# Kernel optimization log

Hardware: AMD Instinct MI355X
Metric: run time of the kernel (lower is better)

Reference implementation:

```python
import jax, jax.numpy as jnp
import numpy as np
from jax import lax

D = 4            # shift radius
NSHIFT = 2 * D + 1  # 9 shifts per axis -> 81 total


def setup_inputs() -> dict:
    key = jax.random.key(0)
    k1, k2, k3, k4, k5, k6 = jax.random.split(key, 6)
    B, C, H, W = 4, 256, 64, 128
    R = 16  # reduction ratio
    feat1 = jax.random.normal(k1, (B, C, H, W), dtype=jnp.float32)
    feat2 = jax.random.normal(k2, (B, C, H, W), dtype=jnp.float32)
    # ca_conv1: Conv2d(C, C//R, 1) -> weight [C//R, C], bias [C//R]
    w1 = jax.random.normal(k3, (C // R, C), dtype=jnp.float32) * (1.0 / np.sqrt(C))
    b1 = jax.random.normal(k4, (C // R,), dtype=jnp.float32) * 0.01
    # ca_conv2: Conv2d(C//R, C, 1) -> weight [C, C//R], bias [C]
    w2 = jax.random.normal(k5, (C, C // R), dtype=jnp.float32) * (1.0 / np.sqrt(C // R))
    b2 = jax.random.normal(k6, (C,), dtype=jnp.float32) * 0.01
    return {"feat1": feat1, "feat2": feat2, "w1": w1, "b1": b1, "w2": w2, "b2": b2}


def reference(feat1, feat2, w1, b1, w2, b2):
    B, C, H, W = feat1.shape
    # zero-pad feat2 spatially by D on each side (matches F.pad constant 0)
    feat2p = jnp.pad(feat2, ((0, 0), (0, 0), (D, D), (D, D)))

    def one_shift(carry, idx):
        i = idx // NSHIFT
        j = idx % NSHIFT
        f2 = lax.dynamic_slice(feat2p, (0, 0, i, j), (B, C, H, W))
        sim = feat1 * f2                              # [B,C,H,W]
        pooled = jnp.mean(sim, axis=(2, 3))           # global avg pool -> [B,C]
        a = pooled @ w1.T + b1                        # [B,C//R] (1x1 conv == matmul)
        a = a @ w2.T + b2                             # [B,C]
        a = jax.nn.sigmoid(a)
        out = jnp.mean(a[:, :, None, None] * sim, axis=1)  # channel mean -> [B,H,W]
        return carry, out

    _, cv = lax.scan(one_shift, None, jnp.arange(NSHIFT * NSHIFT))  # [81,B,H,W]
    return jnp.transpose(cv, (1, 0, 2, 3))  # [B,81,H,W]
```

## Files before the change

kernel.cpp:

```cpp
#include <hip/hip_runtime.h>
#include <math.h>


#define HH 64
#define WW 128
#define CC 256
#define BB 4

__global__ __launch_bounds__(256) void corr_pool_kernel(
    const float* __restrict__ f1, const float* __restrict__ f2,
    float* __restrict__ pooled_part) {
  const int bid   = blockIdx.x;
  const int strip = bid & 1;
  const int bc    = bid >> 1;
  const int h0    = strip << 5;
  const float* f1p = f1 + (size_t)bc * (HH * WW);
  const float* f2p = f2 + (size_t)bc * (HH * WW);

  __shared__ float4 f2s[40 * 35];
  __shared__ float  rowpart[16 * 81];

  const int t = threadIdx.x;
  const float4 z4 = make_float4(0.f, 0.f, 0.f, 0.f);
  for (int u = t; u < 40 * 35; u += 256) {
    const int rl = u / 35, k = u - rl * 35;
    const int gr = h0 - 4 + rl;
    float4 v = z4;
    if ((unsigned)gr < 64u && k >= 1 && k <= 32)
      v = *(const float4*)(f2p + (gr << 7) + ((k - 1) << 2));
    f2s[u] = v;
  }

  const int hl = t >> 3, seg = t & 7, w0 = seg << 4;
  alignas(16) float f1r[16];
#pragma unroll
  for (int m = 0; m < 4; ++m)
    *(float4*)&f1r[4 * m] =
        *(const float4*)(f1p + ((h0 + hl) << 7) + w0 + (m << 2));
  __syncthreads();

  for (int i = 0; i < 9; ++i) {
    alignas(16) float f2r[24];
    const float4* src = &f2s[(hl + i) * 35 + (seg << 2)];
#pragma unroll
    for (int m = 0; m < 6; ++m) *(float4*)&f2r[4 * m] = src[m];

    float s9[9];
#pragma unroll
    for (int j = 0; j < 9; ++j) s9[j] = 0.f;
#pragma unroll
    for (int k = 0; k < 16; ++k) {
      const float a = f1r[k];
#pragma unroll
      for (int j = 0; j < 9; ++j) s9[j] += a * f2r[k + j];
    }
#pragma unroll
    for (int j = 0; j < 9; ++j) {
      s9[j] += __shfl_xor(s9[j], 1);
      s9[j] += __shfl_xor(s9[j], 2);
      s9[j] += __shfl_xor(s9[j], 4);
      s9[j] += __shfl_xor(s9[j], 8);
    }
    if ((t & 15) == 0) {
      const int pr = t >> 4;
#pragma unroll
      for (int j = 0; j < 9; ++j) rowpart[pr * 81 + i * 9 + j] = s9[j];
    }
  }
  __syncthreads();

  if (t < 81) {
    float acc = 0.f;
#pragma unroll
    for (int p = 0; p < 16; ++p) acc += rowpart[p * 81 + t];
    const int b = bc >> 8, c = bc & 255;
    pooled_part[(size_t)strip * 82944 + (size_t)(b * 81 + t) * 256 + c] = acc;
  }
}

__global__ __launch_bounds__(256) void mlp_kernel(
    const float* __restrict__ pooled_part, const float* __restrict__ w1,
    const float* __restrict__ b1, const float* __restrict__ w2,
    const float* __restrict__ b2, float* __restrict__ At) {
  const int bs = blockIdx.x;
  const int t  = threadIdx.x;
  const int b  = bs / 81;
  const int s  = bs - b * 81;
  __shared__ float p[256];
  __shared__ float hid[16];

  p[t] = (pooled_part[(size_t)bs * 256 + t] +
          pooled_part[82944 + (size_t)bs * 256 + t]) * (1.0f / 8192.0f);
  __syncthreads();

  const int g = t >> 4, ln = t & 15;
  float acc = 0.f;
#pragma unroll
  for (int m = 0; m < 16; ++m) {
    const int c = (m << 4) + ln;
    acc += w1[(g << 8) + c] * p[c];
  }
  acc += __shfl_xor(acc, 1);
  acc += __shfl_xor(acc, 2);
  acc += __shfl_xor(acc, 4);
  acc += __shfl_xor(acc, 8);
  if (ln == 0) hid[g] = acc + b1[g];
  __syncthreads();

  float acc2 = b2[t];
#pragma unroll
  for (int k = 0; k < 16; ++k) acc2 += w2[(t << 4) + k] * hid[k];
  const float sv = 1.0f / (1.0f + __expf(-acc2));
  At[((size_t)(b * 256 + t)) * 81 + s] = sv;
}

__global__ __launch_bounds__(64, 4) void out_kernel(
    const float* __restrict__ f1, const float* __restrict__ f2,
    const float* __restrict__ At, float* __restrict__ out,
    float* __restrict__ part) {
  const int bid  = blockIdx.x;
  const int x    = bid & 7;
  const int q    = bid >> 3;
  const int i    = q % 9;
  const int tq   = q / 9;
  const int tile = tq * 8 + x;
  const int half = tile & 1;
  const int rt   = (tile >> 1) & 31;
  const int b    = tile >> 6;
  const int h0   = rt << 1;

  const int t    = threadIdx.x;
  const int r    = t >> 5;
  const int cidx = t & 31;
  const int w0   = cidx << 2;
  const int h    = h0 + r;
  const int hr   = h + i - 4;
  const bool rowok = ((unsigned)hr < 64u);

  float acc[9][4];
#pragma unroll
  for (int j = 0; j < 9; ++j)
#pragma unroll
    for (int k = 0; k < 4; ++k) acc[j][k] = 0.f;

  if (rowok) {
    const int c0 = half << 7;
    const float* p1 = f1 + (size_t)b * (CC * 8192) + (size_t)c0 * 8192 +
                      (h << 7) + w0;
    const float* p2 = f2 + (size_t)b * (CC * 8192) + (size_t)c0 * 8192 +
                      (hr << 7);
    const float* Ab = At + (size_t)b * (CC * 81) + (size_t)c0 * 81 + i * 9;

    const bool vA  = (cidx > 0);
    const bool vC  = (cidx < 31);
    const int ofsA = vA ? (w0 - 4) : 0;
    const int ofsC = vC ? (w0 + 4) : 120;

    float4 nx = *(const float4*)(p1);
    float4 nA = *(const float4*)(p2 + ofsA);
    float4 nB = *(const float4*)(p2 + w0);
    float4 nC = *(const float4*)(p2 + ofsC);

#pragma unroll 4
    for (int c = 0; c < 128; ++c) {
      const float4 xv = nx, fA = nA, fB = nB, fC = nC;
      if (c + 1 < 128) {
        p1 += 8192;
        p2 += 8192;
        nx = *(const float4*)(p1);
        nA = *(const float4*)(p2 + ofsA);
        nB = *(const float4*)(p2 + w0);
        nC = *(const float4*)(p2 + ofsC);
      }

      alignas(16) float f2r[12];
      f2r[0] = vA ? fA.x : 0.f;
      f2r[1] = vA ? fA.y : 0.f;
      f2r[2] = vA ? fA.z : 0.f;
      f2r[3] = vA ? fA.w : 0.f;
      f2r[4] = fB.x; f2r[5] = fB.y; f2r[6] = fB.z; f2r[7] = fB.w;
      f2r[8]  = vC ? fC.x : 0.f;
      f2r[9]  = vC ? fC.y : 0.f;
      f2r[10] = vC ? fC.z : 0.f;
      f2r[11] = vC ? fC.w : 0.f;

      alignas(16) const float xx[4] = {xv.x, xv.y, xv.z, xv.w};

      const float* avp = Ab + (size_t)c * 81;
#pragma unroll
      for (int j = 0; j < 9; ++j) {
        const float wj = avp[j];
#pragma unroll
        for (int k = 0; k < 4; ++k) acc[j][k] += wj * (xx[k] * f2r[k + j]);
      }
    }
  }

  float* dst = half ? part : out;
  const float inv = 1.0f / 256.0f;
#pragma unroll
  for (int j = 0; j < 9; ++j) {
    float4 o;
    o.x = acc[j][0] * inv;
    o.y = acc[j][1] * inv;
    o.z = acc[j][2] * inv;
    o.w = acc[j][3] * inv;
    *(float4*)(dst + (((size_t)(b * 81 + i * 9 + j) * 64 + h) << 7) + w0) = o;
  }
}

__global__ __launch_bounds__(256) void combine_kernel(
    float* __restrict__ out, const float* __restrict__ part) {
  const size_t idx = (size_t)blockIdx.x * 256 + threadIdx.x;
  float4* o4       = (float4*)out;
  const float4* p4 = (const float4*)part;
  const float4 a = o4[idx], p = p4[idx];
  float4 rv;
  rv.x = a.x + p.x; rv.y = a.y + p.y; rv.z = a.z + p.z; rv.w = a.w + p.w;
  o4[idx] = rv;
}

extern "C" void kernel_launch(void* const* d_in, const int* in_sizes, int n_in,
                              void* d_out, int out_size, void* d_ws, size_t ws_size,
                              hipStream_t stream) {
  const float* feat1 = (const float*)d_in[0];
  const float* feat2 = (const float*)d_in[1];
  const float* w1    = (const float*)d_in[2];
  const float* b1    = (const float*)d_in[3];
  const float* w2    = (const float*)d_in[4];
  const float* b2    = (const float*)d_in[5];
  float* out = (float*)d_out;

  float* pooled_part = (float*)d_ws;
  float* At          = pooled_part + 2 * 82944;
  float* cpart       = At + 82944;

  corr_pool_kernel<<<2048, 256, 0, stream>>>(feat1, feat2, pooled_part);
  mlp_kernel<<<4 * 81, 256, 0, stream>>>(pooled_part, w1, b1, w2, b2, At);
  out_kernel<<<2304, 64, 0, stream>>>(feat1, feat2, At, out, cpart);
  combine_kernel<<<2592, 256, 0, stream>>>(out, cpart);
}
```

Baseline: 217.9 us.

## Restructure correlation pooling to one block per channel with row-shift thread mapping

The pooling kernel now processes a whole (batch, channel) plane per block of 576 threads, where each thread owns one row and one vertical shift and accumulates 9 horizontal shifts over all width segments. This removes the per-shift shuffle reductions and the two-strip partial buffer, so the MLP kernel reads a single pooled array. f1 is now read from global memory by 9 threads per row instead of once, and shared memory grows to hold the full padded f2 plane, which may limit occupancy. The output kernel's prefetch loop is also made branchless by clamping the pointer advance, and its unroll pragma is removed.

```diff
diff --git a/kernel.cpp b/kernel.cpp
--- a/kernel.cpp
+++ b/kernel.cpp
@@ -7,79 +7,73 @@
 #define CC 256
 #define BB 4
 
-__global__ __launch_bounds__(256) void corr_pool_kernel(
+__global__ __launch_bounds__(576, 6) void corr_pool_kernel(
     const float* __restrict__ f1, const float* __restrict__ f2,
-    float* __restrict__ pooled_part) {
-  const int bid   = blockIdx.x;
-  const int strip = bid & 1;
-  const int bc    = bid >> 1;
-  const int h0    = strip << 5;
+    float* __restrict__ pooled) {
+  const int t  = threadIdx.x;
+  const int bc = blockIdx.x;
   const float* f1p = f1 + (size_t)bc * (HH * WW);
   const float* f2p = f2 + (size_t)bc * (HH * WW);
 
-  __shared__ float4 f2s[40 * 35];
-  __shared__ float  rowpart[16 * 81];
-
-  const int t = threadIdx.x;
+  __shared__ float4 f2s4[72 * 35];
+  float* red = (float*)f2s4;
+
   const float4 z4 = make_float4(0.f, 0.f, 0.f, 0.f);
-  for (int u = t; u < 40 * 35; u += 256) {
+  for (int u = t; u < 72 * 35; u += 576) {
     const int rl = u / 35, k = u - rl * 35;
-    const int gr = h0 - 4 + rl;
+    const int gr = rl - 4;
     float4 v = z4;
     if ((unsigned)gr < 64u && k >= 1 && k <= 32)
       v = *(const float4*)(f2p + (gr << 7) + ((k - 1) << 2));
-    f2s[u] = v;
-  }
-
-  const int hl = t >> 3, seg = t & 7, w0 = seg << 4;
-  alignas(16) float f1r[16];
-#pragma unroll
-  for (int m = 0; m < 4; ++m)
-    *(float4*)&f1r[4 * m] =
-        *(const float4*)(f1p + ((h0 + hl) << 7) + w0 + (m << 2));
-  __syncthreads();
-
-  for (int i = 0; i < 9; ++i) {
-    alignas(16) float f2r[24];
-    const float4* src = &f2s[(hl + i) * 35 + (seg << 2)];
-#pragma unroll
-    for (int m = 0; m < 6; ++m) *(float4*)&f2r[4 * m] = src[m];
-
-    float s9[9];
-#pragma unroll
-    for (int j = 0; j < 9; ++j) s9[j] = 0.f;
+    f2s4[u] = v;
+  }
+  __syncthreads();
+
+  const int h  = t / 9;
+  const int di = t - h * 9;
+  const float4* f2row = &f2s4[(h + di) * 35];
+  const float* f1row  = f1p + (h << 7);
+
+  float s9[9];
+#pragma unroll
+  for (int j = 0; j < 9; ++j) s9[j] = 0.f;
+
+#pragma unroll 2
+  for (int seg = 0; seg < 8; ++seg) {
+    const int w0 = seg << 4;
+    alignas(16) float f1r[16];
+#pragma unroll
+    for (int m = 0; m < 4; ++m)
+      *(float4*)&f1r[4 * m] = *(const float4*)(f1row + w0 + (m << 2));
+
+    alignas(16) float f2w[24];
+#pragma unroll
+    for (int m = 0; m < 6; ++m) *(float4*)&f2w[4 * m] = f2row[(seg << 2) + m];
+
 #pragma unroll
     for (int k = 0; k < 16; ++k) {
       const float a = f1r[k];
 #pragma unroll
-      for (int j = 0; j < 9; ++j) s9[j] += a * f2r[k + j];
+      for (int j = 0; j < 9; ++j) s9[j] += a * f2w[k + j];
     }
-#pragma unroll
-    for (int j = 0; j < 9; ++j) {
-      s9[j] += __shfl_xor(s9[j], 1);
-      s9[j] += __shfl_xor(s9[j], 2);
-      s9[j] += __shfl_xor(s9[j], 4);
-      s9[j] += __shfl_xor(s9[j], 8);
-    }
-    if ((t & 15) == 0) {
-      const int pr = t >> 4;
-#pragma unroll
-      for (int j = 0; j < 9; ++j) rowpart[pr * 81 + i * 9 + j] = s9[j];
-    }
-  }
+  }
+
+  __syncthreads();
+#pragma unroll
+  for (int j = 0; j < 9; ++j) red[h * 81 + di * 9 + j] = s9[j];
   __syncthreads();
 
   if (t < 81) {
     float acc = 0.f;
-#pragma unroll
-    for (int p = 0; p < 16; ++p) acc += rowpart[p * 81 + t];
+#pragma unroll 8
+    for (int hh = 0; hh < 64; ++hh) acc += red[hh * 81 + t];
     const int b = bc >> 8, c = bc & 255;
-    pooled_part[(size_t)strip * 82944 + (size_t)(b * 81 + t) * 256 + c] = acc;
+    pooled[(size_t)(b * 81 + t) * 256 + c] = acc;
   }
 }
 
 __global__ __launch_bounds__(256) void mlp_kernel(
-    const float* __restrict__ pooled_part, const float* __restrict__ w1,
+    const float* __restrict__ pooled, const float* __restrict__ w1,
     const float* __restrict__ b1, const float* __restrict__ w2,
     const float* __restrict__ b2, float* __restrict__ At) {
   const int bs = blockIdx.x;
@@ -89,8 +83,7 @@
   __shared__ float p[256];
   __shared__ float hid[16];
 
-  p[t] = (pooled_part[(size_t)bs * 256 + t] +
-          pooled_part[82944 + (size_t)bs * 256 + t]) * (1.0f / 8192.0f);
+  p[t] = pooled[(size_t)bs * 256 + t] * (1.0f / 8192.0f);
   __syncthreads();
 
   const int g = t >> 4, ln = t & 15;
@@ -161,17 +154,15 @@
     float4 nB = *(const float4*)(p2 + w0);
     float4 nC = *(const float4*)(p2 + ofsC);
 
-#pragma unroll 4
     for (int c = 0; c < 128; ++c) {
       const float4 xv = nx, fA = nA, fB = nB, fC = nC;
-      if (c + 1 < 128) {
-        p1 += 8192;
-        p2 += 8192;
-        nx = *(const float4*)(p1);
-        nA = *(const float4*)(p2 + ofsA);
-        nB = *(const float4*)(p2 + w0);
-        nC = *(const float4*)(p2 + ofsC);
-      }
+      const int adv = (c < 127) ? 8192 : 0;
+      p1 += adv;
+      p2 += adv;
+      nx = *(const float4*)(p1);
+      nA = *(const float4*)(p2 + ofsA);
+      nB = *(const float4*)(p2 + w0);
+      nC = *(const float4*)(p2 + ofsC);
 
       alignas(16) float f2r[12];
       f2r[0] = vA ? fA.x : 0.f;
@@ -231,12 +222,12 @@
   const float* b2    = (const float*)d_in[5];
   float* out = (float*)d_out;
 
-  float* pooled_part = (float*)d_ws;
-  float* At          = pooled_part + 2 * 82944;
-  float* cpart       = At + 82944;
-
-  corr_pool_kernel<<<2048, 256, 0, stream>>>(feat1, feat2, pooled_part);
-  mlp_kernel<<<4 * 81, 256, 0, stream>>>(pooled_part, w1, b1, w2, b2, At);
+  float* pooled = (float*)d_ws;
+  float* At     = pooled + 82944;
+  float* cpart  = At + 82944;
+
+  corr_pool_kernel<<<1024, 576, 0, stream>>>(feat1, feat2, pooled);
+  mlp_kernel<<<4 * 81, 256, 0, stream>>>(pooled, w1, b1, w2, b2, At);
   out_kernel<<<2304, 64, 0, stream>>>(feat1, feat2, At, out, cpart);
   combine_kernel<<<2592, 256, 0, stream>>>(out, cpart);
 }
```

New measurement: 195.9 us. 1.11x faster.
